# Kernel tuning notes

Measured on AMD Instinct MI355X. Metric: run time of the kernel, lower is better.

## Reference

```python
import jax, jax.numpy as jnp
import numpy as np

ROI, P = 28, 7          # ROI window on feature map; output grid 7x7 -> 4x4 bins
BIN = ROI // P
C, CLASSES = 64, 2      # channels after vgg features[:2]; n classes
H = W = 512
N_ROI = 2000
D_FC = 4096


def setup_inputs() -> dict:
    key = jax.random.key(0)
    k = jax.random.split(key, 8)
    s = 0.02
    return {
        "img": jax.random.normal(k[0], (3, H, W), jnp.float32),
        "regions": jax.random.randint(k[1], (N_ROI, 2), 0, H - ROI, jnp.int32),
        "conv_w": jax.random.normal(k[2], (C, 3, 3, 3), jnp.float32) * s,
        "conv_b": jnp.zeros((C,), jnp.float32),
        "fc1_w": jax.random.normal(k[3], (D_FC, C * P * P), jnp.float32) * s,
        "fc1_b": jnp.zeros((D_FC,), jnp.float32),
        "fc2_w": jax.random.normal(k[4], (D_FC, D_FC), jnp.float32) * s,
        "fc2_b": jnp.zeros((D_FC,), jnp.float32),
        "cls_w": jax.random.normal(k[5], (CLASSES, D_FC), jnp.float32) * s,
        "cls_b": jnp.zeros((CLASSES,), jnp.float32),
        "bbox_w": jax.random.normal(k[6], (CLASSES * 4, D_FC), jnp.float32) * s,
        "bbox_b": jnp.zeros((CLASSES * 4,), jnp.float32),
    }


def reference(img, regions, conv_w, conv_b, fc1_w, fc1_b,
              fc2_w, fc2_b, cls_w, cls_b, bbox_w, bbox_b):
    # conv trunk: vgg16.features[:2] = Conv2d(3,64,3,pad=1) + ReLU
    fmap = jax.lax.conv_general_dilated(
        img[None], conv_w, window_strides=(1, 1), padding="SAME",
        dimension_numbers=("NCHW", "OIHW", "NCHW"))[0]
    fmap = jax.nn.relu(fmap + conv_b[:, None, None])        # [C, H, W]

    # per-region crop (irregular gather), vectorized over regions
    def crop(rc):
        return jax.lax.dynamic_slice(fmap, (0, rc[0], rc[1]), (C, ROI, ROI))
    rois = jax.vmap(crop)(regions)                          # [N, C, ROI, ROI]

    # RoI max pooling: divide ROIxROI window into PxP grid, max each bin
    pooled = rois.reshape(N_ROI, C, P, BIN, P, BIN).max(axis=(3, 5))  # [N,C,P,P]
    feat = pooled.reshape(N_ROI, C * P * P)

    # vgg classifier[:-1] (Dropout = identity at inference)
    feat = jax.nn.relu(feat @ fc1_w.T + fc1_b)
    feat = jax.nn.relu(feat @ fc2_w.T + fc2_b)              # [N, 4096]

    cls_logits = feat @ cls_w.T + cls_b                     # [N, CLASSES]
    loc_bbox = feat @ bbox_w.T + bbox_b                     # [N, CLASSES*4]
    return (cls_logits, loc_bbox)
```

## Files before the change

kernel.cpp:

```cpp
#include <hip/hip_runtime.h>

typedef unsigned short u16;
typedef unsigned int u32;
using bf16x8 = __attribute__((ext_vector_type(8))) short;
using f32x4  = __attribute__((ext_vector_type(4))) float;
using ushort8 = __attribute__((ext_vector_type(8))) unsigned short;

__device__ __forceinline__ u16 f2bf(float f) {
  u32 u = __float_as_uint(f);
  return (u16)((u + 0x7FFFu + ((u >> 16) & 1u)) >> 16);
}
__device__ __forceinline__ float bf2f(u16 h) {
  return __uint_as_float(((u32)h) << 16);
}
__device__ __forceinline__ ushort8 umax8(ushort8 a, ushort8 b) {
  return __builtin_elementwise_max(a, b);
}

__global__ __launch_bounds__(256) void conv3x3_relu_k(
    const float* __restrict__ img, const float* __restrict__ w,
    const float* __restrict__ bias, u16* __restrict__ fmap) {
  int p = blockIdx.x * 256 + threadIdx.x;
  int y = p >> 9, x = p & 511;
  float v[27];
#pragma unroll
  for (int ci = 0; ci < 3; ++ci)
#pragma unroll
    for (int ky = 0; ky < 3; ++ky)
#pragma unroll
      for (int kx = 0; kx < 3; ++kx) {
        int yy = y + ky - 1, xx = x + kx - 1;
        bool ok = (yy >= 0) && (yy < 512) && (xx >= 0) && (xx < 512);
        v[(ci * 3 + ky) * 3 + kx] = ok ? img[ci * 262144 + yy * 512 + xx] : 0.f;
      }
  float acc[64];
#pragma unroll
  for (int co = 0; co < 64; ++co) {
    float s = bias[co];
#pragma unroll
    for (int q = 0; q < 27; ++q) s = fmaf(w[co * 27 + q], v[q], s);
    acc[co] = fmaxf(s, 0.f);
  }
  uint4* dst = (uint4*)((u32*)fmap + (size_t)p * 32);
#pragma unroll
  for (int q = 0; q < 8; ++q) {
    uint4 d;
    d.x = (u32)f2bf(acc[8 * q + 0]) | ((u32)f2bf(acc[8 * q + 1]) << 16);
    d.y = (u32)f2bf(acc[8 * q + 2]) | ((u32)f2bf(acc[8 * q + 3]) << 16);
    d.z = (u32)f2bf(acc[8 * q + 4]) | ((u32)f2bf(acc[8 * q + 5]) << 16);
    d.w = (u32)f2bf(acc[8 * q + 6]) | ((u32)f2bf(acc[8 * q + 7]) << 16);
    dst[q] = d;
  }
}

__global__ __launch_bounds__(256) void vmax_k(
    const u16* __restrict__ fmap, u16* __restrict__ M1) {
  int g = blockIdx.x * 256 + threadIdx.x;
  int cg = g & 7, x = (g >> 3) & 511, ych = g >> 12;
  int y0 = ych * 64;
  ushort8 h0, h1, h2;
  for (int i = 0; i < 67; ++i) {
    int yy = y0 + i; if (yy > 511) yy = 511;
    ushort8 r = *(const ushort8*)(fmap + (((size_t)(yy * 512 + x)) << 6) + cg * 8);
    if (i >= 3) {
      ushort8 m = umax8(umax8(h0, h1), umax8(h2, r));
      *(ushort8*)(M1 + (((size_t)((y0 + i - 3) * 512 + x)) << 6) + cg * 8) = m;
    }
    h0 = h1; h1 = h2; h2 = r;
  }
}

__global__ __launch_bounds__(256) void roipool2_k(
    const u16* __restrict__ M1, const int* __restrict__ regions,
    u16* __restrict__ feat) {
  int n = blockIdx.x, t = threadIdx.x;
  uint4* fdst = (uint4*)(feat + (size_t)n * 3136);
  if (n >= 2000) {
    uint4 z; z.x = z.y = z.z = z.w = 0u;
    for (int w = t; w < 392; w += 256) fdst[w] = z;
    return;
  }
  __shared__ u16 frow[3136];
  int r0 = regions[2 * n], c0 = regions[2 * n + 1];
  for (int w = t; w < 392; w += 256) {
    int bin = w >> 3, cg = w & 7;
    int py = bin / 7, px = bin % 7;
    int y = r0 + py * 4, xb = c0 + px * 4;
    const u16* base = M1 + (((size_t)(y * 512 + xb)) << 6) + cg * 8;
    ushort8 a = *(const ushort8*)(base);
    ushort8 b = *(const ushort8*)(base + 64);
    ushort8 c = *(const ushort8*)(base + 128);
    ushort8 d = *(const ushort8*)(base + 192);
    ushort8 m = umax8(umax8(a, b), umax8(c, d));
#pragma unroll
    for (int k = 0; k < 8; ++k) frow[(cg * 8 + k) * 49 + bin] = m[k];
  }
  __syncthreads();
  const uint4* fsrc = (const uint4*)frow;
  for (int w = t; w < 392; w += 256) fdst[w] = fsrc[w];
}

__global__ __launch_bounds__(256) void f2bf_k(const float* __restrict__ in,
                                              u16* __restrict__ out, int n4) {
  int idx = blockIdx.x * 256 + threadIdx.x;
  int stride = gridDim.x * 256;
  for (int i = idx; i < n4; i += stride) {
    float4 v = ((const float4*)in)[i];
    uint2 o;
    o.x = (u32)f2bf(v.x) | ((u32)f2bf(v.y) << 16);
    o.y = (u32)f2bf(v.z) | ((u32)f2bf(v.w) << 16);
    ((uint2*)out)[i] = o;
  }
}

__global__ __launch_bounds__(512, 2) void gemm8_bt_relu_k(
    const u16* __restrict__ A, const u16* __restrict__ B,
    const float* __restrict__ bias, u16* __restrict__ C, int N, int K) {
  __shared__ uint4 lds4[9216];
  char* ldsb = (char*)lds4;
  const int t = threadIdx.x;
  const int lane = t & 63, wv = t >> 6;
  const int wm = wv >> 2, wn = wv & 3;

  int bid = blockIdx.x;
  int swz = ((bid & 7) << 5) | (bid >> 3);
  const int nb = swz >> 4, mb = swz & 15;
  const int m0 = mb * 128, n0 = nb * 256;

  const u16* __restrict__ Ab = A + (size_t)m0 * K;
  const u16* __restrict__ Bb = B + (size_t)n0 * K;

  const int srow = t >> 3;
  const int sslot = (t & 7) ^ (srow & 7);
  const u16* pA0 = Ab + (size_t)srow * K + sslot * 8;
  const u16* pA1 = pA0 + (size_t)64 * K;
  const u16* pB0 = Bb + (size_t)srow * K + sslot * 8;
  const u16* pB1 = pB0 + (size_t)64 * K;
  const u16* pB2 = pB0 + (size_t)128 * K;
  const u16* pB3 = pB0 + (size_t)192 * K;
  const int dof = t * 16;

#define G2L(src, ldst)                                                        \
  __builtin_amdgcn_global_load_lds(                                          \
      (const __attribute__((address_space(1))) void*)(src),                  \
      (__attribute__((address_space(3))) void*)(ldst), 16, 0, 0)

  const int rA = wm * 64 + (lane & 15);
  const int rB = wn * 64 + (lane & 15);
  const int sl = lane >> 4;
#define LOFF(r, slot) (((r) << 7) + ((((slot) ^ ((r) & 7))) << 4))

  f32x4 acc[4][4] = {};
  bf16x8 afr[4][2], bfr[4][2];

  const int NT = K >> 6;
  {
    char* A0 = ldsb; char* B0 = A0 + 16384;
    char* A1 = ldsb + 49152; char* B1 = A1 + 16384;
    G2L(pA0, A0 + dof); G2L(pA1, A0 + 8192 + dof);
    G2L(pB0, B0 + dof); G2L(pB1, B0 + 8192 + dof);
    G2L(pB2, B0 + 16384 + dof); G2L(pB3, B0 + 24576 + dof);
    G2L(pA0 + 64, A1 + dof); G2L(pA1 + 64, A1 + 8192 + dof);
    G2L(pB0 + 64, B1 + dof); G2L(pB1 + 64, B1 + 8192 + dof);
    G2L(pB2 + 64, B1 + 16384 + dof); G2L(pB3 + 64, B1 + 24576 + dof);
  }
  asm volatile("s_waitcnt vmcnt(6)" ::: "memory");
  __builtin_amdgcn_s_barrier();

  int cb = 0;
  for (int tt = 0; tt < NT; ++tt) {
    const int pb = (cb + 2 >= 3) ? cb - 1 : cb + 2;
    const bool pf = (tt + 2) < NT;
    char* Acur = ldsb + cb * 49152; char* Bcur = Acur + 16384;
    char* Apf  = ldsb + pb * 49152; char* Bpf  = Apf + 16384;
    const int kof = (tt + 2) << 6;

    if (pf) {
      G2L(pA0 + kof, Apf + dof);
      G2L(pA1 + kof, Apf + 8192 + dof);
      G2L(pB0 + kof, Bpf + dof);
      G2L(pB1 + kof, Bpf + 8192 + dof);
      G2L(pB2 + kof, Bpf + 16384 + dof);
      G2L(pB3 + kof, Bpf + 24576 + dof);
    }
    __builtin_amdgcn_sched_barrier(0);
    __builtin_amdgcn_s_setprio(1);
#pragma unroll
    for (int j = 0; j < 4; ++j) {
      bfr[j][0] = *(const bf16x8*)(Bcur + LOFF(rB + j * 16, sl));
      bfr[j][1] = *(const bf16x8*)(Bcur + LOFF(rB + j * 16, 4 + sl));
    }
#pragma unroll
    for (int i = 0; i < 4; ++i) {
      afr[i][0] = *(const bf16x8*)(Acur + LOFF(rA + i * 16, sl));
      afr[i][1] = *(const bf16x8*)(Acur + LOFF(rA + i * 16, 4 + sl));
    }
#pragma unroll
    for (int i = 0; i < 4; ++i)
#pragma unroll
      for (int j = 0; j < 4; ++j) {
        acc[i][j] = __builtin_amdgcn_mfma_f32_16x16x32_bf16(afr[i][0], bfr[j][0], acc[i][j], 0, 0, 0);
        acc[i][j] = __builtin_amdgcn_mfma_f32_16x16x32_bf16(afr[i][1], bfr[j][1], acc[i][j], 0, 0, 0);
      }
    __builtin_amdgcn_s_setprio(0);
    if (pf) {
      asm volatile("s_waitcnt vmcnt(6)" ::: "memory");
    } else if (tt + 1 < NT) {
      asm volatile("s_waitcnt vmcnt(0)" ::: "memory");
    }
    __builtin_amdgcn_s_barrier();
    cb = (cb == 2) ? 0 : cb + 1;
  }
#undef G2L
#undef LOFF

  float bv[4];
#pragma unroll
  for (int j = 0; j < 4; ++j) bv[j] = bias[n0 + wn * 64 + j * 16 + (lane & 15)];
#pragma unroll
  for (int i = 0; i < 4; ++i)
#pragma unroll
    for (int j = 0; j < 4; ++j) {
      int cg = n0 + wn * 64 + j * 16 + (lane & 15);
#pragma unroll
      for (int r = 0; r < 4; ++r) {
        int rg = m0 + wm * 64 + i * 16 + (lane >> 4) * 4 + r;
        float v = fmaxf(acc[i][j][r] + bv[j], 0.f);
        C[(size_t)rg * N + cg] = f2bf(v);
      }
    }
}

__global__ __launch_bounds__(256) void heads_k(
    const u16* __restrict__ h2, const float* __restrict__ cw,
    const float* __restrict__ cb, const float* __restrict__ bw,
    const float* __restrict__ bb, float* __restrict__ out) {
  int m = blockIdx.x, t = threadIdx.x;
  const u16* hrow = h2 + (size_t)m * 4096;
  float p[10];
#pragma unroll
  for (int j = 0; j < 10; ++j) p[j] = 0.f;
  for (int k = t; k < 4096; k += 256) {
    float v = bf2f(hrow[k]);
    p[0] = fmaf(v, cw[k], p[0]);
    p[1] = fmaf(v, cw[4096 + k], p[1]);
#pragma unroll
    for (int j = 0; j < 8; ++j) p[2 + j] = fmaf(v, bw[j * 4096 + k], p[2 + j]);
  }
#pragma unroll
  for (int j = 0; j < 10; ++j)
#pragma unroll
    for (int off = 32; off > 0; off >>= 1) p[j] += __shfl_down(p[j], off);
  __shared__ float red[4][10];
  int lane = t & 63, wv = t >> 6;
  if (lane == 0) {
#pragma unroll
    for (int j = 0; j < 10; ++j) red[wv][j] = p[j];
  }
  __syncthreads();
  if (t < 10) {
    float s = red[0][t] + red[1][t] + red[2][t] + red[3][t];
    s += (t < 2) ? cb[t] : bb[t - 2];
    if (t < 2) out[m * 2 + t] = s;
    else out[4000 + m * 8 + (t - 2)] = s;
  }
}

extern "C" void kernel_launch(void* const* d_in, const int* in_sizes, int n_in,
                              void* d_out, int out_size, void* d_ws, size_t ws_size,
                              hipStream_t stream) {
  const float* img    = (const float*)d_in[0];
  const int*   regions= (const int*)d_in[1];
  const float* conv_w = (const float*)d_in[2];
  const float* conv_b = (const float*)d_in[3];
  const float* fc1_w  = (const float*)d_in[4];
  const float* fc1_b  = (const float*)d_in[5];
  const float* fc2_w  = (const float*)d_in[6];
  const float* fc2_b  = (const float*)d_in[7];
  const float* cls_w  = (const float*)d_in[8];
  const float* cls_b  = (const float*)d_in[9];
  const float* bbox_w = (const float*)d_in[10];
  const float* bbox_b = (const float*)d_in[11];
  float* out = (float*)d_out;

  char* ws = (char*)d_ws;
  u16* fmap = (u16*)(ws);
  u16* h1   = (u16*)(ws);
  u16* h2   = (u16*)(ws + 16777216);
  u16* M1   = (u16*)(ws + 33554432);
  u16* w2b  = (u16*)(ws + 33554432);
  u16* feat = (u16*)(ws + 67108864);
  u16* w1b  = (u16*)(ws + 79953920);

  conv3x3_relu_k<<<1024, 256, 0, stream>>>(img, conv_w, conv_b, fmap);
  vmax_k<<<128, 256, 0, stream>>>(fmap, M1);
  roipool2_k<<<2048, 256, 0, stream>>>(M1, regions, feat);
  f2bf_k<<<2048, 256, 0, stream>>>(fc1_w, w1b, 4096 * 3136 / 4);
  f2bf_k<<<2048, 256, 0, stream>>>(fc2_w, w2b, 4096 * 4096 / 4);
  gemm8_bt_relu_k<<<256, 512, 0, stream>>>(feat, w1b, fc1_b, h1, 4096, 3136);
  gemm8_bt_relu_k<<<256, 512, 0, stream>>>(h1, w2b, fc2_b, h2, 4096, 4096);
  heads_k<<<2000, 256, 0, stream>>>(h2, cls_w, cls_b, bbox_w, bbox_b, out);
}
```

Before: 224.9 us.

## Fuse conv with vertical max, merge weight casts, batch heads with LDS weights

The 3x3 conv+ReLU is fused with the 4-row vertical max. Each thread keeps a rolling 3-row input window and a 4-row output history, so the full bf16 feature map is never written or re-read. The two fp32-to-bf16 weight conversions become one launch. The heads kernel now stages the cls/bbox weights as bf16 in shared memory and loops over 8 rows per block. The trade-offs are extra conv recomputation at the 3-row halos of each 8-row band, bf16 rounding of the head weights, and more register pressure in the conv.

```diff
diff --git a/kernel.cpp b/kernel.cpp
--- a/kernel.cpp
+++ b/kernel.cpp
@@ -17,57 +17,92 @@
   return __builtin_elementwise_max(a, b);
 }
 
-__global__ __launch_bounds__(256) void conv3x3_relu_k(
+__global__ __launch_bounds__(512) void conv_vmax_k(
     const float* __restrict__ img, const float* __restrict__ w,
-    const float* __restrict__ bias, u16* __restrict__ fmap) {
-  int p = blockIdx.x * 256 + threadIdx.x;
-  int y = p >> 9, x = p & 511;
-  float v[27];
-#pragma unroll
-  for (int ci = 0; ci < 3; ++ci)
-#pragma unroll
-    for (int ky = 0; ky < 3; ++ky)
+    const float* __restrict__ bias, u16* __restrict__ M1) {
+  const int t = threadIdx.x;
+  const int x = ((blockIdx.x & 15) << 5) + (t >> 4);
+  const int cq = (t & 15) << 2;
+  const int y0 = (blockIdx.x >> 4) << 3;
+
+  float wr[27][4];
+#pragma unroll
+  for (int p = 0; p < 27; ++p)
+#pragma unroll
+    for (int c = 0; c < 4; ++c) wr[p][c] = w[(cq + c) * 27 + p];
+  float bz[4];
+#pragma unroll
+  for (int c = 0; c < 4; ++c) bz[c] = bias[cq + c];
+
+  const bool xm = (x > 0), xp = (x < 511);
+  float win[3][3][3];
+
+#define LOADROW(yy, s)                                                        \
+  do {                                                                        \
+    if ((yy) >= 0 && (yy) <= 511) {                                          \
+      _Pragma("unroll") for (int ci = 0; ci < 3; ++ci) {                      \
+        const float* rp = img + ci * 262144 + (yy) * 512 + x;                 \
+        win[ci][s][0] = xm ? rp[-1] : 0.f;                                    \
+        win[ci][s][1] = rp[0];                                                \
+        win[ci][s][2] = xp ? rp[1] : 0.f;                                     \
+      }                                                                        \
+    } else {                                                                   \
+      _Pragma("unroll") for (int ci = 0; ci < 3; ++ci) {                      \
+        win[ci][s][0] = 0.f; win[ci][s][1] = 0.f; win[ci][s][2] = 0.f;        \
+      }                                                                        \
+    }                                                                          \
+  } while (0)
+
+  LOADROW(y0 - 1, 0);
+  LOADROW(y0, 1);
+
+  float h0[4], h1[4], h2[4], cur[4];
+#pragma unroll
+  for (int i = 0; i < 11; ++i) {
+    const int r = y0 + i;
+    LOADROW(r + 1, 2);
+    if (r <= 511) {
+#pragma unroll
+      for (int c = 0; c < 4; ++c) cur[c] = bz[c];
+#pragma unroll
+      for (int ci = 0; ci < 3; ++ci)
+#pragma unroll
+        for (int ky = 0; ky < 3; ++ky)
+#pragma unroll
+          for (int kx = 0; kx < 3; ++kx) {
+            const float iv = win[ci][ky][kx];
+            const int p = ci * 9 + ky * 3 + kx;
+#pragma unroll
+            for (int c = 0; c < 4; ++c) cur[c] = fmaf(wr[p][c], iv, cur[c]);
+          }
+#pragma unroll
+      for (int c = 0; c < 4; ++c) cur[c] = fmaxf(cur[c], 0.f);
+    } else {
+#pragma unroll
+      for (int c = 0; c < 4; ++c) cur[c] = 0.f;
+    }
+    if (i >= 3) {
+      const int ym = r - 3;
+      float m[4];
+#pragma unroll
+      for (int c = 0; c < 4; ++c)
+        m[c] = fmaxf(fmaxf(h0[c], h1[c]), fmaxf(h2[c], cur[c]));
+      uint2 o;
+      o.x = (u32)f2bf(m[0]) | ((u32)f2bf(m[1]) << 16);
+      o.y = (u32)f2bf(m[2]) | ((u32)f2bf(m[3]) << 16);
+      *(uint2*)(M1 + (((size_t)(ym * 512 + x)) << 6) + cq) = o;
+    }
+#pragma unroll
+    for (int c = 0; c < 4; ++c) { h0[c] = h1[c]; h1[c] = h2[c]; h2[c] = cur[c]; }
+#pragma unroll
+    for (int ci = 0; ci < 3; ++ci)
 #pragma unroll
       for (int kx = 0; kx < 3; ++kx) {
-        int yy = y + ky - 1, xx = x + kx - 1;
-        bool ok = (yy >= 0) && (yy < 512) && (xx >= 0) && (xx < 512);
-        v[(ci * 3 + ky) * 3 + kx] = ok ? img[ci * 262144 + yy * 512 + xx] : 0.f;
+        win[ci][0][kx] = win[ci][1][kx];
+        win[ci][1][kx] = win[ci][2][kx];
       }
-  float acc[64];
-#pragma unroll
-  for (int co = 0; co < 64; ++co) {
-    float s = bias[co];
-#pragma unroll
-    for (int q = 0; q < 27; ++q) s = fmaf(w[co * 27 + q], v[q], s);
-    acc[co] = fmaxf(s, 0.f);
-  }
-  uint4* dst = (uint4*)((u32*)fmap + (size_t)p * 32);
-#pragma unroll
-  for (int q = 0; q < 8; ++q) {
-    uint4 d;
-    d.x = (u32)f2bf(acc[8 * q + 0]) | ((u32)f2bf(acc[8 * q + 1]) << 16);
-    d.y = (u32)f2bf(acc[8 * q + 2]) | ((u32)f2bf(acc[8 * q + 3]) << 16);
-    d.z = (u32)f2bf(acc[8 * q + 4]) | ((u32)f2bf(acc[8 * q + 5]) << 16);
-    d.w = (u32)f2bf(acc[8 * q + 6]) | ((u32)f2bf(acc[8 * q + 7]) << 16);
-    dst[q] = d;
-  }
-}
-
-__global__ __launch_bounds__(256) void vmax_k(
-    const u16* __restrict__ fmap, u16* __restrict__ M1) {
-  int g = blockIdx.x * 256 + threadIdx.x;
-  int cg = g & 7, x = (g >> 3) & 511, ych = g >> 12;
-  int y0 = ych * 64;
-  ushort8 h0, h1, h2;
-  for (int i = 0; i < 67; ++i) {
-    int yy = y0 + i; if (yy > 511) yy = 511;
-    ushort8 r = *(const ushort8*)(fmap + (((size_t)(yy * 512 + x)) << 6) + cg * 8);
-    if (i >= 3) {
-      ushort8 m = umax8(umax8(h0, h1), umax8(h2, r));
-      *(ushort8*)(M1 + (((size_t)((y0 + i - 3) * 512 + x)) << 6) + cg * 8) = m;
-    }
-    h0 = h1; h1 = h2; h2 = r;
-  }
+  }
+#undef LOADROW
 }
 
 __global__ __launch_bounds__(256) void roipool2_k(
@@ -100,16 +135,20 @@
   for (int w = t; w < 392; w += 256) fdst[w] = fsrc[w];
 }
 
-__global__ __launch_bounds__(256) void f2bf_k(const float* __restrict__ in,
-                                              u16* __restrict__ out, int n4) {
+__global__ __launch_bounds__(256) void f2bf2_k(
+    const float* __restrict__ in1, u16* __restrict__ out1, int n4a,
+    const float* __restrict__ in2, u16* __restrict__ out2, int n4total) {
   int idx = blockIdx.x * 256 + threadIdx.x;
   int stride = gridDim.x * 256;
-  for (int i = idx; i < n4; i += stride) {
-    float4 v = ((const float4*)in)[i];
+  for (int i = idx; i < n4total; i += stride) {
+    const float* in; u16* o16; int k;
+    if (i < n4a) { in = in1; o16 = out1; k = i; }
+    else         { in = in2; o16 = out2; k = i - n4a; }
+    float4 v = ((const float4*)in)[k];
     uint2 o;
     o.x = (u32)f2bf(v.x) | ((u32)f2bf(v.y) << 16);
     o.y = (u32)f2bf(v.z) | ((u32)f2bf(v.w) << 16);
-    ((uint2*)out)[i] = o;
+    ((uint2*)o16)[k] = o;
   }
 }
 
@@ -235,34 +274,57 @@
     const u16* __restrict__ h2, const float* __restrict__ cw,
     const float* __restrict__ cb, const float* __restrict__ bw,
     const float* __restrict__ bb, float* __restrict__ out) {
-  int m = blockIdx.x, t = threadIdx.x;
-  const u16* hrow = h2 + (size_t)m * 4096;
-  float p[10];
-#pragma unroll
-  for (int j = 0; j < 10; ++j) p[j] = 0.f;
-  for (int k = t; k < 4096; k += 256) {
-    float v = bf2f(hrow[k]);
-    p[0] = fmaf(v, cw[k], p[0]);
-    p[1] = fmaf(v, cw[4096 + k], p[1]);
-#pragma unroll
-    for (int j = 0; j < 8; ++j) p[2 + j] = fmaf(v, bw[j * 4096 + k], p[2 + j]);
-  }
-#pragma unroll
-  for (int j = 0; j < 10; ++j)
-#pragma unroll
-    for (int off = 32; off > 0; off >>= 1) p[j] += __shfl_down(p[j], off);
+  __shared__ u16 wl[10][4096];
   __shared__ float red[4][10];
-  int lane = t & 63, wv = t >> 6;
-  if (lane == 0) {
-#pragma unroll
-    for (int j = 0; j < 10; ++j) red[wv][j] = p[j];
+  const int t = threadIdx.x;
+  for (int i4 = t; i4 < 10240; i4 += 256) {
+    int j = i4 >> 10, k4 = i4 & 1023;
+    float4 v = (j < 2) ? ((const float4*)cw)[j * 1024 + k4]
+                       : ((const float4*)bw)[(j - 2) * 1024 + k4];
+    uint2 o;
+    o.x = (u32)f2bf(v.x) | ((u32)f2bf(v.y) << 16);
+    o.y = (u32)f2bf(v.z) | ((u32)f2bf(v.w) << 16);
+    *(uint2*)(&wl[j][k4 * 4]) = o;
   }
   __syncthreads();
-  if (t < 10) {
-    float s = red[0][t] + red[1][t] + red[2][t] + red[3][t];
-    s += (t < 2) ? cb[t] : bb[t - 2];
-    if (t < 2) out[m * 2 + t] = s;
-    else out[4000 + m * 8 + (t - 2)] = s;
+  const int lane = t & 63, wvi = t >> 6;
+  const int m0 = blockIdx.x * 8;
+  for (int mi = 0; mi < 8; ++mi) {
+    const int m = m0 + mi;
+    const u16* hrow = h2 + (size_t)m * 4096;
+    float p[10];
+#pragma unroll
+    for (int j = 0; j < 10; ++j) p[j] = 0.f;
+#pragma unroll
+    for (int h = 0; h < 2; ++h) {
+      const int kc = t + h * 256;
+      ushort8 hv = ((const ushort8*)hrow)[kc];
+      float hf[8];
+#pragma unroll
+      for (int e = 0; e < 8; ++e) hf[e] = bf2f(hv[e]);
+#pragma unroll
+      for (int j = 0; j < 10; ++j) {
+        ushort8 wv = *(const ushort8*)(&wl[j][kc * 8]);
+#pragma unroll
+        for (int e = 0; e < 8; ++e) p[j] = fmaf(hf[e], bf2f(wv[e]), p[j]);
+      }
+    }
+#pragma unroll
+    for (int j = 0; j < 10; ++j)
+#pragma unroll
+      for (int off = 32; off > 0; off >>= 1) p[j] += __shfl_down(p[j], off);
+    if (lane == 0) {
+#pragma unroll
+      for (int j = 0; j < 10; ++j) red[wvi][j] = p[j];
+    }
+    __syncthreads();
+    if (t < 10) {
+      float s = red[0][t] + red[1][t] + red[2][t] + red[3][t];
+      s += (t < 2) ? cb[t] : bb[t - 2];
+      if (t < 2) out[m * 2 + t] = s;
+      else out[4000 + m * 8 + (t - 2)] = s;
+    }
+    __syncthreads();
   }
 }
 
@@ -284,20 +346,17 @@
   float* out = (float*)d_out;
 
   char* ws = (char*)d_ws;
-  u16* fmap = (u16*)(ws);
+  u16* M1   = (u16*)(ws);
   u16* h1   = (u16*)(ws);
   u16* h2   = (u16*)(ws + 16777216);
-  u16* M1   = (u16*)(ws + 33554432);
-  u16* w2b  = (u16*)(ws + 33554432);
-  u16* feat = (u16*)(ws + 67108864);
-  u16* w1b  = (u16*)(ws + 79953920);
-
-  conv3x3_relu_k<<<1024, 256, 0, stream>>>(img, conv_w, conv_b, fmap);
-  vmax_k<<<128, 256, 0, stream>>>(fmap, M1);
+  u16* feat = (u16*)(ws + 33554432);
+  u16* w1b  = (u16*)(ws + 46399488);
+  u16* w2b  = (u16*)(ws + 72089600);
+
+  conv_vmax_k<<<1024, 512, 0, stream>>>(img, conv_w, conv_b, M1);
   roipool2_k<<<2048, 256, 0, stream>>>(M1, regions, feat);
-  f2bf_k<<<2048, 256, 0, stream>>>(fc1_w, w1b, 4096 * 3136 / 4);
-  f2bf_k<<<2048, 256, 0, stream>>>(fc2_w, w2b, 4096 * 4096 / 4);
+  f2bf2_k<<<2048, 256, 0, stream>>>(fc1_w, w1b, 3211264, fc2_w, w2b, 7405568);
   gemm8_bt_relu_k<<<256, 512, 0, stream>>>(feat, w1b, fc1_b, h1, 4096, 3136);
   gemm8_bt_relu_k<<<256, 512, 0, stream>>>(h1, w2b, fc2_b, h2, 4096, 4096);
-  heads_k<<<2000, 256, 0, stream>>>(h2, cls_w, cls_b, bbox_w, bbox_b, out);
-}
+  heads_k<<<250, 256, 0, stream>>>(h2, cls_w, cls_b, bbox_w, bbox_b, out);
+}
```

New measurement: 222.7 us. About the same (-1.0%).
